# Performance work log

Hardware: AMD Instinct MI355X
Metric: run time of the kernel (lower is better)

Reference implementation:

```python
import jax, jax.numpy as jnp
import numpy as np

B, SQ, SK, H = 8, 2048, 2048, 256
NH, HD = 4, 64  # num_heads, head_dim


def setup_inputs() -> dict:
    key = jax.random.key(0)
    ks = jax.random.split(key, 9)
    scale = 0.02
    inp = {
        'query': jax.random.normal(ks[0], (B, SQ, H), jnp.float32),
        'key':   jax.random.normal(ks[1], (B, SK, H), jnp.float32),
        'value': jax.random.normal(ks[2], (B, SK, H), jnp.float32),
        'mask':  jax.random.bernoulli(ks[3], 0.9, (B, SQ, SK)),
        'Wq': jax.random.normal(ks[4], (H, H), jnp.float32) * scale,
        'bq': jnp.zeros((H,), jnp.float32),
        'Wk': jax.random.normal(ks[5], (H, H), jnp.float32) * scale,
        'bk': jnp.zeros((H,), jnp.float32),
        'Wv': jax.random.normal(ks[6], (H, H), jnp.float32) * scale,
        'bv': jnp.zeros((H,), jnp.float32),
        'Wo': jax.random.normal(ks[7], (H, H), jnp.float32) * scale,
        'bo': jnp.zeros((H,), jnp.float32),
    }
    return inp


def reference(query, key, value, mask, Wq, bq, Wk, bk, Wv, bv, Wo, bo):
    b = query.shape[0]
    scale = jnp.asarray(HD, query.dtype) ** -0.5
    # torch Linear: x @ W.T + b; reshape to [B, NH, S, HD]
    Q = (query @ Wq.T + bq).reshape(b, -1, NH, HD).transpose(0, 2, 1, 3)
    K = (key   @ Wk.T + bk).reshape(b, -1, NH, HD).transpose(0, 2, 1, 3)
    V = (value @ Wv.T + bv).reshape(b, -1, NH, HD).transpose(0, 2, 1, 3)
    scores = jnp.einsum('bhqd,bhkd->bhqk', Q, K) * scale  # [B,NH,SQ,SK]
    # mask-fixing: rows with no valid key get key 0 unmasked
    mask_sum = mask.sum(axis=-1)  # [B,SQ]
    mask_fixed = mask.at[:, :, 0].set(jnp.where(mask_sum == 0, True, mask[:, :, 0]))
    scores = jnp.where(mask_fixed[:, None, :, :], scores, jnp.asarray(-1e9, scores.dtype))
    attn = jax.nn.softmax(scores, axis=-1)
    attn = jnp.where(jnp.isnan(attn), jnp.zeros_like(attn), attn)  # NaN fix
    out = jnp.einsum('bhqk,bhkd->bhqd', attn, V)
    out = out.transpose(0, 2, 1, 3).reshape(b, -1, H)
    out = out @ Wo.T + bo
    return out, attn
```

## Files before the change

### kernel.cpp

```cpp
#include <hip/hip_runtime.h>
#include <math.h>

#define Bn  8
#define SQn 2048
#define SKn 2048
#define Hn  256
#define NHn 4
#define HDn 64
#define SCALE2 0.1803368801111f

typedef __attribute__((ext_vector_type(4))) float f32x4;
typedef __attribute__((ext_vector_type(4))) unsigned int u32x4;
typedef __attribute__((ext_vector_type(8))) short short8;
typedef unsigned short ushort_t;
typedef unsigned long long ull_t;

__device__ __forceinline__ unsigned short f2bf(float f) {
  unsigned u = __builtin_bit_cast(unsigned, f);
  u += 0x7fffu + ((u >> 16) & 1u);
  return (unsigned short)(u >> 16);
}

__device__ __forceinline__ float fexp2(float x) {
  return __builtin_amdgcn_exp2f(x);
}

__device__ __forceinline__ float bf2f(unsigned short v) {
  unsigned u = (unsigned)v << 16;
  return __builtin_bit_cast(float, u);
}

__device__ __forceinline__ short8 load8f(const float* p) {
  float4 v0 = *(const float4*)p;
  float4 v1 = *(const float4*)(p + 4);
  short8 r;
  r[0] = (short)f2bf(v0.x); r[1] = (short)f2bf(v0.y);
  r[2] = (short)f2bf(v0.z); r[3] = (short)f2bf(v0.w);
  r[4] = (short)f2bf(v1.x); r[5] = (short)f2bf(v1.y);
  r[6] = (short)f2bf(v1.z); r[7] = (short)f2bf(v1.w);
  return r;
}

__device__ __forceinline__ f32x4 mfma16(short8 a, short8 b, f32x4 c) {
  return __builtin_amdgcn_mfma_f32_16x16x32_bf16(a, b, c, 0, 0, 0);
}

__global__ __launch_bounds__(256) void prep_kernel(
    const void* __restrict__ maskp,
    const float* __restrict__ Wq, const float* __restrict__ Wk,
    const float* __restrict__ Wv, const float* __restrict__ Wo,
    ull_t* __restrict__ mout, ushort_t* __restrict__ Wb)
{
  const int bid = blockIdx.x;
  if (bid < 16) {
    const int g = bid * 256 + threadIdx.x;
    #pragma unroll
    for (int it = 0; it < 8; ++it) {
      const int grp = g + it * 4096;
      const int w = grp >> 13;
      const int off = (grp & 8191) * 8;
      const float* src = w == 0 ? Wq : w == 1 ? Wk : w == 2 ? Wv : Wo;
      *(short8*)(Wb + w * 65536 + off) = load8f(src + off);
    }
    return;
  }
  const int l = threadIdx.x & 63;
  const unsigned probe = ((const unsigned*)maskp)[l];
  const int isbyte = __any(probe > 1u);
  const int gwave = ((bid - 16) * 256 + threadIdx.x) >> 6;
  const int nwaves = (gridDim.x - 16) * 4;
  const long long total4 = (long long)Bn * SQn * (SKn / 256);
  if (isbyte) {
    for (long long w = gwave; w < total4; w += nwaves) {
      const unsigned char* mp = (const unsigned char*)maskp + w * 256;
      bool n0 = mp[l] != 0,        n1 = mp[64 + l] != 0;
      bool n2 = mp[128 + l] != 0,  n3 = mp[192 + l] != 0;
      ull_t b0 = __ballot(n0), b1 = __ballot(n1);
      ull_t b2 = __ballot(n2), b3 = __ballot(n3);
      if (l == 0) {
        mout[w * 4] = b0; mout[w * 4 + 1] = b1;
        mout[w * 4 + 2] = b2; mout[w * 4 + 3] = b3;
      }
    }
  } else {
    for (long long w = gwave; w < total4; w += nwaves) {
      const int* mp = (const int*)maskp + w * 256;
      bool n0 = mp[l] != 0,        n1 = mp[64 + l] != 0;
      bool n2 = mp[128 + l] != 0,  n3 = mp[192 + l] != 0;
      ull_t b0 = __ballot(n0), b1 = __ballot(n1);
      ull_t b2 = __ballot(n2), b3 = __ballot(n3);
      if (l == 0) {
        mout[w * 4] = b0; mout[w * 4 + 1] = b1;
        mout[w * 4 + 2] = b2; mout[w * 4 + 3] = b3;
      }
    }
  }
}

__global__ __launch_bounds__(256) void proj3_kernel(
    const float* __restrict__ Xq, const float* __restrict__ Xk,
    const float* __restrict__ Xv, const ushort_t* __restrict__ Wb,
    const float* __restrict__ bqp, const float* __restrict__ bkp,
    const float* __restrict__ bvp,
    ushort_t* __restrict__ Qb, ushort_t* __restrict__ Kb,
    ushort_t* __restrict__ Vt)
{
  const int which = blockIdx.z;
  const float* X = which == 0 ? Xq : which == 1 ? Xk : Xv;
  const ushort_t* W = Wb + which * 65536;
  const float* bias = which == 0 ? bqp : which == 1 ? bkp : bvp;
  ushort_t* Y = which == 0 ? Qb : which == 1 ? Kb : Vt;
  const int vtrans = (which == 2);

  const int m0 = blockIdx.x * 64;
  const int n0 = blockIdx.y * 64;
  const int wv = threadIdx.x >> 6;
  const int l  = threadIdx.x & 63;
  const int lr = l & 15, lg = l >> 4;
  const int mrow = m0 + wv * 16 + lr;

  f32x4 acc[4];
  #pragma unroll
  for (int t = 0; t < 4; ++t) acc[t] = (f32x4){0.f, 0.f, 0.f, 0.f};

  const float* ap = X + (size_t)mrow * Hn + lg * 8;
  for (int k0 = 0; k0 < Hn; k0 += 32) {
    short8 a = load8f(ap + k0);
    #pragma unroll
    for (int t = 0; t < 4; ++t) {
      short8 bb = *(const short8*)(W + (size_t)(n0 + t * 16 + lr) * Hn + k0 + lg * 8);
      acc[t] = mfma16(a, bb, acc[t]);
    }
  }

  #pragma unroll
  for (int t = 0; t < 4; ++t) {
    const int n = n0 + t * 16 + lr;
    const float bv = bias[n];
    const int h = n >> 6, d = n & 63;
    if (!vtrans) {
      #pragma unroll
      for (int r = 0; r < 4; ++r) {
        const int m = m0 + wv * 16 + lg * 4 + r;
        const int bb = m >> 11, s = m & 2047;
        size_t idx = (((size_t)bb * NHn + h) * SQn + s) * HDn + d;
        Y[idx] = f2bf(acc[t][r] + bv);
      }
    } else {
      const int m = m0 + wv * 16 + lg * 4;
      const int bb = m >> 11, s = m & 2047;
      ushort4 pk;
      pk.x = f2bf(acc[t][0] + bv); pk.y = f2bf(acc[t][1] + bv);
      pk.z = f2bf(acc[t][2] + bv); pk.w = f2bf(acc[t][3] + bv);
      size_t idx = (((size_t)bb * NHn + h) * HDn + d) * (size_t)SKn + s;
      *(ushort4*)(Y + idx) = pk;
    }
  }
}

__global__ __launch_bounds__(512)
__attribute__((amdgpu_waves_per_eu(4, 4)))
void fused_attn_kernel(
    const ushort_t* __restrict__ Qb, const ushort_t* __restrict__ Kb,
    const ushort_t* __restrict__ Vt, const unsigned* __restrict__ maskbits,
    float* __restrict__ attn_out, ushort_t* __restrict__ Ob)
{
  __shared__ float red[8][16];
  __shared__ float Opart[8][16][66];

  const int bid = blockIdx.x;
  const int rt = (bid & 7) * 512 + (bid >> 3);
  const int wv = threadIdx.x >> 6;
  const int l  = threadIdx.x & 63;
  const int lr = l & 15, lg = l >> 4;
  const int bh = rt >> 7;
  const int q0 = (rt & 127) << 4;
  const int b  = bh >> 2, h = bh & 3;
  const int colbase = wv * 256;

  const ushort_t* Qh = Qb + (size_t)bh * SQn * HDn;
  const ushort_t* Kh = Kb + (size_t)bh * SKn * HDn;
  const ushort_t* Vh = Vt + (size_t)bh * HDn * SKn;

  short8 qa0 = *(const short8*)(Qh + (q0 + lr) * HDn + lg * 8);
  short8 qa1 = *(const short8*)(Qh + (q0 + lr) * HDn + 32 + lg * 8);

  const int krA = (lr >> 2) * 8 + (lr & 3);
  const unsigned* mrow = maskbits + ((size_t)b * SQn + q0 + lr) * (SKn / 32) + wv * 8;
  const int bsh = lg * 8;

  short8 pf8[8];
  float lsum = 0.f;
  f32x4 oacc[4];
  #pragma unroll
  for (int dt = 0; dt < 4; ++dt) oacc[dt] = (f32x4){0.f, 0.f, 0.f, 0.f};

  u32x4 mw = *(const u32x4*)mrow;
  #pragma unroll
  for (int s8 = 0; s8 < 8; ++s8) {
    if (s8 == 4) mw = *(const u32x4*)(mrow + 4);
    const int c = colbase + s8 * 32;
    const ushort_t* kp = Kh + (size_t)(c + krA) * HDn + lg * 8;
    short8 ka0 = *(const short8*)(kp);
    short8 ka1 = *(const short8*)(kp + 32);
    short8 kb0 = *(const short8*)(kp + 4 * HDn);
    short8 kb1 = *(const short8*)(kp + 4 * HDn + 32);
    f32x4 za = (f32x4){0.f, 0.f, 0.f, 0.f}, zb = (f32x4){0.f, 0.f, 0.f, 0.f};
    za = mfma16(ka0, qa0, za); za = mfma16(ka1, qa1, za);
    zb = mfma16(kb0, qa0, zb); zb = mfma16(kb1, qa1, zb);

    const ushort_t* vp = Vh + (size_t)lr * SKn + c + lg * 8;
    short8 vb0 = *(const short8*)(vp);
    short8 vb1 = *(const short8*)(vp + 16 * SKn);
    short8 vb2 = *(const short8*)(vp + 32 * SKn);
    short8 vb3 = *(const short8*)(vp + 48 * SKn);

    const unsigned bits = (mw[s8 & 3] >> bsh) & 0xFFu;
    short8 pf;
    #pragma unroll
    for (int j = 0; j < 4; ++j) {
      float pa = ((bits >> j) & 1) ? fexp2(za[j] * SCALE2) : 0.f;
      float pb = ((bits >> (4 + j)) & 1) ? fexp2(zb[j] * SCALE2) : 0.f;
      lsum += pa + pb;
      pf[j] = (short)f2bf(pa);
      pf[4 + j] = (short)f2bf(pb);
    }
    pf8[s8] = pf;
    oacc[0] = mfma16(pf, vb0, oacc[0]);
    oacc[1] = mfma16(pf, vb1, oacc[1]);
    oacc[2] = mfma16(pf, vb2, oacc[2]);
    oacc[3] = mfma16(pf, vb3, oacc[3]);
  }

  lsum += __shfl_xor(lsum, 16);
  lsum += __shfl_xor(lsum, 32);
  if (l < 16) red[wv][lr] = lsum;
  #pragma unroll
  for (int dt = 0; dt < 4; ++dt)
    #pragma unroll
    for (int r = 0; r < 4; ++r)
      Opart[wv][lg * 4 + r][dt * 16 + lr] = oacc[dt][r];
  __syncthreads();

  float gsum = 0.f;
  #pragma unroll
  for (int ww = 0; ww < 8; ++ww) gsum += red[ww][lr];
  const bool rowempty = (gsum == 0.f);
  const float rinv = rowempty ? 0.f : 1.f / gsum;

  float* arow = attn_out + ((size_t)bh * SQn + q0 + lr) * (size_t)SKn;
  #pragma unroll
  for (int s8 = 0; s8 < 8; ++s8) {
    const int c = colbase + s8 * 32;
    float av[8];
    #pragma unroll
    for (int j = 0; j < 8; ++j)
      av[j] = bf2f((unsigned short)pf8[s8][j]) * rinv;
    if (rowempty && s8 == 0 && wv == 0 && lg == 0) av[0] = 1.f;
    *(f32x4*)(arow + c + lg * 8)     = (f32x4){av[0], av[1], av[2], av[3]};
    *(f32x4*)(arow + c + lg * 8 + 4) = (f32x4){av[4], av[5], av[6], av[7]};
  }

  #pragma unroll
  for (int e = threadIdx.x; e < 1024; e += 512) {
    const int row = e >> 6, d = e & 63;
    float gs = 0.f;
    #pragma unroll
    for (int ww = 0; ww < 8; ++ww) gs += red[ww][row];
    float s = 0.f;
    #pragma unroll
    for (int ww = 0; ww < 8; ++ww) s += Opart[ww][row][d];
    float val;
    if (gs == 0.f) {
      val = bf2f(Vh[(size_t)d * SKn]);
    } else {
      val = s / gs;
    }
    Ob[((size_t)b * SQn + q0 + row) * Hn + h * HDn + d] = f2bf(val);
  }
}

__global__ __launch_bounds__(256) void oproj_kernel(
    const unsigned short* __restrict__ A, const ushort_t* __restrict__ Wob,
    const float* __restrict__ bias, float* __restrict__ out)
{
  const int m0 = blockIdx.x * 64;
  const int n0 = blockIdx.y * 64;
  const int wv = threadIdx.x >> 6;
  const int l  = threadIdx.x & 63;
  const int lr = l & 15, lg = l >> 4;
  const int mrow = m0 + wv * 16 + lr;

  f32x4 acc[4];
  #pragma unroll
  for (int t = 0; t < 4; ++t) acc[t] = (f32x4){0.f, 0.f, 0.f, 0.f};

  for (int k0 = 0; k0 < Hn; k0 += 32) {
    short8 a = *(const short8*)(A + (size_t)mrow * Hn + k0 + lg * 8);
    #pragma unroll
    for (int t = 0; t < 4; ++t) {
      short8 bb = *(const short8*)(Wob + (size_t)(n0 + t * 16 + lr) * Hn + k0 + lg * 8);
      acc[t] = mfma16(a, bb, acc[t]);
    }
  }
  #pragma unroll
  for (int t = 0; t < 4; ++t) {
    const int n = n0 + t * 16 + lr;
    const float bv = bias[n];
    #pragma unroll
    for (int r = 0; r < 4; ++r) {
      const int m = m0 + wv * 16 + lg * 4 + r;
      out[(size_t)m * Hn + n] = acc[t][r] + bv;
    }
  }
}

extern "C" void kernel_launch(void* const* d_in, const int* in_sizes, int n_in,
                              void* d_out, int out_size, void* d_ws, size_t ws_size,
                              hipStream_t stream) {
  const float* query = (const float*)d_in[0];
  const float* key_  = (const float*)d_in[1];
  const float* value = (const float*)d_in[2];
  const void*  mask  = d_in[3];
  const float* Wq = (const float*)d_in[4];
  const float* bq = (const float*)d_in[5];
  const float* Wk = (const float*)d_in[6];
  const float* bk = (const float*)d_in[7];
  const float* Wv = (const float*)d_in[8];
  const float* bv = (const float*)d_in[9];
  const float* Wo = (const float*)d_in[10];
  const float* bo = (const float*)d_in[11];

  float* out  = (float*)d_out;
  float* attn = out + (size_t)Bn * SQn * Hn;

  char* ws = (char*)d_ws;
  unsigned short* Qb = (unsigned short*)ws;
  unsigned short* Kb = Qb + (size_t)Bn * SQn * Hn;
  unsigned short* Vt = Kb + (size_t)Bn * SKn * Hn;
  unsigned short* Ob = Vt + (size_t)Bn * SKn * Hn;
  unsigned* mbits = (unsigned*)(Ob + (size_t)Bn * SQn * Hn);
  ushort_t* Wb = (ushort_t*)(mbits + (size_t)Bn * SQn * (SKn / 32));

  prep_kernel<<<1040, 256, 0, stream>>>(mask, Wq, Wk, Wv, Wo,
                                        (ull_t*)mbits, Wb);
  proj3_kernel<<<dim3(256, 4, 3), 256, 0, stream>>>(
      query, key_, value, Wb, bq, bk, bv, Qb, Kb, Vt);
  fused_attn_kernel<<<4096, 512, 0, stream>>>(Qb, Kb, Vt, mbits, attn, Ob);
  oproj_kernel<<<dim3(256, 4), 256, 0, stream>>>(Ob, Wb + 3 * 65536, bo, out);
}
```

Baseline: 459.3 us.

## Stage unnormalized probabilities in attn output to free registers, raise waves per EU

Instead of holding eight bf16 probability fragments per lane in registers until the row sum is known, the kernel writes unnormalized fp32 probabilities straight to the attention output buffer. It then reads them back, scales them by the inverse sum and writes them again. Freeing those registers lets the occupancy hint rise from 4 to 6 waves per EU. The cost is doubled global write traffic plus an extra read of the 128 MB attention matrix, which is the dominant memory cost. As a side effect, precision improves because the stored values are fp32 rather than bf16-rounded.

```diff
diff --git a/kernel.cpp b/kernel.cpp
--- a/kernel.cpp
+++ b/kernel.cpp
@@ -159,7 +159,7 @@
 }
 
 __global__ __launch_bounds__(512)
-__attribute__((amdgpu_waves_per_eu(4, 4)))
+__attribute__((amdgpu_waves_per_eu(6, 6)))
 void fused_attn_kernel(
     const ushort_t* __restrict__ Qb, const ushort_t* __restrict__ Kb,
     const ushort_t* __restrict__ Vt, const unsigned* __restrict__ maskbits,
@@ -189,7 +189,8 @@
   const unsigned* mrow = maskbits + ((size_t)b * SQn + q0 + lr) * (SKn / 32) + wv * 8;
   const int bsh = lg * 8;
 
-  short8 pf8[8];
+  float* arow = attn_out + ((size_t)bh * SQn + q0 + lr) * (size_t)SKn;
+
   float lsum = 0.f;
   f32x4 oacc[4];
   #pragma unroll
@@ -216,16 +217,24 @@
     short8 vb3 = *(const short8*)(vp + 48 * SKn);
 
     const unsigned bits = (mw[s8 & 3] >> bsh) & 0xFFu;
+    float pa0 = ((bits >> 0) & 1) ? fexp2(za[0] * SCALE2) : 0.f;
+    float pa1 = ((bits >> 1) & 1) ? fexp2(za[1] * SCALE2) : 0.f;
+    float pa2 = ((bits >> 2) & 1) ? fexp2(za[2] * SCALE2) : 0.f;
+    float pa3 = ((bits >> 3) & 1) ? fexp2(za[3] * SCALE2) : 0.f;
+    float pb0 = ((bits >> 4) & 1) ? fexp2(zb[0] * SCALE2) : 0.f;
+    float pb1 = ((bits >> 5) & 1) ? fexp2(zb[1] * SCALE2) : 0.f;
+    float pb2 = ((bits >> 6) & 1) ? fexp2(zb[2] * SCALE2) : 0.f;
+    float pb3 = ((bits >> 7) & 1) ? fexp2(zb[3] * SCALE2) : 0.f;
+    lsum += (pa0 + pa1 + pa2 + pa3) + (pb0 + pb1 + pb2 + pb3);
+
+    *(f32x4*)(arow + c + lg * 8)     = (f32x4){pa0, pa1, pa2, pa3};
+    *(f32x4*)(arow + c + lg * 8 + 4) = (f32x4){pb0, pb1, pb2, pb3};
+
     short8 pf;
-    #pragma unroll
-    for (int j = 0; j < 4; ++j) {
-      float pa = ((bits >> j) & 1) ? fexp2(za[j] * SCALE2) : 0.f;
-      float pb = ((bits >> (4 + j)) & 1) ? fexp2(zb[j] * SCALE2) : 0.f;
-      lsum += pa + pb;
-      pf[j] = (short)f2bf(pa);
-      pf[4 + j] = (short)f2bf(pb);
-    }
-    pf8[s8] = pf;
+    pf[0] = (short)f2bf(pa0); pf[1] = (short)f2bf(pa1);
+    pf[2] = (short)f2bf(pa2); pf[3] = (short)f2bf(pa3);
+    pf[4] = (short)f2bf(pb0); pf[5] = (short)f2bf(pb1);
+    pf[6] = (short)f2bf(pb2); pf[7] = (short)f2bf(pb3);
     oacc[0] = mfma16(pf, vb0, oacc[0]);
     oacc[1] = mfma16(pf, vb1, oacc[1]);
     oacc[2] = mfma16(pf, vb2, oacc[2]);
@@ -248,17 +257,16 @@
   const bool rowempty = (gsum == 0.f);
   const float rinv = rowempty ? 0.f : 1.f / gsum;
 
-  float* arow = attn_out + ((size_t)bh * SQn + q0 + lr) * (size_t)SKn;
   #pragma unroll
   for (int s8 = 0; s8 < 8; ++s8) {
     const int c = colbase + s8 * 32;
-    float av[8];
-    #pragma unroll
-    for (int j = 0; j < 8; ++j)
-      av[j] = bf2f((unsigned short)pf8[s8][j]) * rinv;
-    if (rowempty && s8 == 0 && wv == 0 && lg == 0) av[0] = 1.f;
-    *(f32x4*)(arow + c + lg * 8)     = (f32x4){av[0], av[1], av[2], av[3]};
-    *(f32x4*)(arow + c + lg * 8 + 4) = (f32x4){av[4], av[5], av[6], av[7]};
+    f32x4 wa = *(const f32x4*)(arow + c + lg * 8);
+    f32x4 wb = *(const f32x4*)(arow + c + lg * 8 + 4);
+    #pragma unroll
+    for (int j = 0; j < 4; ++j) { wa[j] *= rinv; wb[j] *= rinv; }
+    if (rowempty && s8 == 0 && wv == 0 && lg == 0) wa[0] = 1.f;
+    *(f32x4*)(arow + c + lg * 8)     = wa;
+    *(f32x4*)(arow + c + lg * 8 + 4) = wb;
   }
 
   #pragma unroll
```

Result: slower. 569.6 us (+24.0%).
